# Performance work log

Hardware: AMD Instinct MI355X
Metric: run time of the kernel (lower is better)

The kernel has to match this reference:

```python
import jax, jax.numpy as jnp
import numpy as np

DIM = 1024
NUM_HEADS = 16
HEAD_DIM = DIM // NUM_HEADS
SCALE = HEAD_DIM ** -0.5
CAUSAL = True


def setup_inputs() -> dict:
    key = jax.random.key(0)
    k_x, k_qkv, k_proj, k_pb = jax.random.split(key, 4)
    B, S = 4, 2048
    x = jax.random.normal(k_x, (B, S, DIM), dtype=jnp.float32)
    # nn.Linear(dim, 3*dim, bias=False): weight [3*dim, dim]; store transposed [dim, 3*dim]
    w_qkv = jax.random.normal(k_qkv, (DIM, 3 * DIM), dtype=jnp.float32) * (DIM ** -0.5)
    w_proj = jax.random.normal(k_proj, (DIM, DIM), dtype=jnp.float32) * (DIM ** -0.5)
    b_proj = jax.random.normal(k_pb, (DIM,), dtype=jnp.float32) * 0.01
    return {"x": x, "w_qkv": w_qkv, "w_proj": w_proj, "b_proj": b_proj}


def reference(x, w_qkv, w_proj, b_proj):
    B, S, C = x.shape
    # qkv: [B, S, 3, H, D] -> q,k,v each [B, H, S, D]
    qkv = (x @ w_qkv).reshape(B, S, 3, NUM_HEADS, HEAD_DIM)
    qkv = jnp.transpose(qkv, (2, 0, 3, 1, 4))
    q, k, v = qkv[0], qkv[1], qkv[2]
    # scores [B, H, S, S]
    attn = jnp.einsum('bhqd,bhkd->bhqk', q, k) * SCALE
    if CAUSAL:
        causal_mask = jnp.triu(jnp.ones((S, S), dtype=bool), k=1)
        attn = jnp.where(causal_mask, -jnp.inf, attn)
    attn = jax.nn.softmax(attn, axis=-1)
    out = jnp.einsum('bhqk,bhkd->bhqd', attn, v)
    out = jnp.transpose(out, (0, 2, 1, 3)).reshape(B, S, C)
    return out @ w_proj + b_proj
```

## Files before the change

kernel.cpp:

```cpp
#include <hip/hip_runtime.h>
#include <hip/hip_bf16.h>
#include <math.h>

#define DIMC 1024
#define NHEADS 16
#define HDIM 64
#define BATCH 4
#define SEQ 2048
#define NROWS (BATCH * SEQ)
#define ATTN_SCALE 0.125f
#define LOG2E 1.4426950408889634f

typedef __attribute__((ext_vector_type(8))) short short8;
typedef __attribute__((ext_vector_type(4))) short short4v;
typedef __attribute__((ext_vector_type(4))) float f32x4;

static __device__ __forceinline__ short f2bf(float f) {
    __hip_bfloat16 h = __float2bfloat16(f);
    return *reinterpret_cast<short*>(&h);
}

static __device__ __forceinline__ void gload16(const void* g, void* l) {
    __builtin_amdgcn_global_load_lds(
        (const __attribute__((address_space(1))) unsigned int*)g,
        (__attribute__((address_space(3))) unsigned int*)l, 16, 0, 0);
}

__global__ __launch_bounds__(256)
void xcvt(const float* __restrict__ in, unsigned short* __restrict__ out) {
    int i = blockIdx.x * 256 + threadIdx.x;
    const float4* p = reinterpret_cast<const float4*>(in) + 2 * i;
    float4 a = p[0], b = p[1];
    short8 pk;
    pk[0] = f2bf(a.x); pk[1] = f2bf(a.y); pk[2] = f2bf(a.z); pk[3] = f2bf(a.w);
    pk[4] = f2bf(b.x); pk[5] = f2bf(b.y); pk[6] = f2bf(b.z); pk[7] = f2bf(b.w);
    reinterpret_cast<short8*>(out)[i] = pk;
}

__global__ __launch_bounds__(256)
void transpose_cvt(const float* __restrict__ src, unsigned short* __restrict__ dst,
                   int N) {
    __shared__ float t[64][65];
    const int tid = threadIdx.x;
    const int cb = blockIdx.x * 64;
    const int rb = blockIdx.y * 64;
#pragma unroll
    for (int e = 0; e < 4; e++) {
        int idx = tid + e * 256;
        int row = idx >> 4;
        int c4 = (idx & 15) << 2;
        *reinterpret_cast<float4*>(&t[row][c4]) =
            *reinterpret_cast<const float4*>(&src[(size_t)(rb + row) * N + cb + c4]);
    }
    __syncthreads();
#pragma unroll
    for (int e = 0; e < 2; e++) {
        int idx = tid + e * 256;
        int col = idx >> 3;
        int k8 = (idx & 7) << 3;
        short8 pk;
#pragma unroll
        for (int j = 0; j < 8; j++) pk[j] = f2bf(t[k8 + j][col]);
        *reinterpret_cast<short8*>(&dst[(size_t)(cb + col) * 1024 + rb + k8]) = pk;
    }
}

__global__ __launch_bounds__(256)
void qkv_gemm_mfma(const unsigned short* __restrict__ Xbf,
                   const unsigned short* __restrict__ Wt,
                   unsigned short* __restrict__ qo, unsigned short* __restrict__ ko,
                   unsigned short* __restrict__ vt) {
    __shared__ short Alds[128][32];
    __shared__ short Blds[128][32];
    const int tid = threadIdx.x;
    const int lane = tid & 63;
    const int wave = tid >> 6;
    const int wr = wave >> 1, wc = wave & 1;
    const int rowbase = blockIdx.y * 128;
    const int colbase = blockIdx.x * 128;
    const int g = lane >> 4, li = lane & 15;
    const int srow0 = (wave * 2 + 0) * 16 + (lane >> 2);
    const int srow1 = (wave * 2 + 1) * 16 + (lane >> 2);
    const int scol = (lane & 3) * 8;
    short* aflat = &Alds[0][0];
    short* bflat = &Blds[0][0];

    f32x4 acc[4][4];
#pragma unroll
    for (int m = 0; m < 4; m++)
#pragma unroll
        for (int n = 0; n < 4; n++) acc[m][n] = (f32x4){0.f, 0.f, 0.f, 0.f};

    for (int k0 = 0; k0 < DIMC; k0 += 32) {
        gload16(&Xbf[(size_t)(rowbase + srow0) * DIMC + k0 + scol],
                aflat + (wave * 2 + 0) * 512);
        gload16(&Xbf[(size_t)(rowbase + srow1) * DIMC + k0 + scol],
                aflat + (wave * 2 + 1) * 512);
        gload16(&Wt[(size_t)(colbase + srow0) * 1024 + k0 + scol],
                bflat + (wave * 2 + 0) * 512);
        gload16(&Wt[(size_t)(colbase + srow1) * 1024 + k0 + scol],
                bflat + (wave * 2 + 1) * 512);
        __syncthreads();
        short8 af[4], bfr[4];
#pragma unroll
        for (int m = 0; m < 4; m++)
            af[m] = *reinterpret_cast<const short8*>(&Alds[wr * 64 + m * 16 + li][g * 8]);
#pragma unroll
        for (int n = 0; n < 4; n++)
            bfr[n] = *reinterpret_cast<const short8*>(&Blds[wc * 64 + n * 16 + li][g * 8]);
#pragma unroll
        for (int m = 0; m < 4; m++)
#pragma unroll
            for (int n = 0; n < 4; n++)
                acc[m][n] = __builtin_amdgcn_mfma_f32_16x16x32_bf16(
                    af[m], bfr[n], acc[m][n], 0, 0, 0);
        __syncthreads();
    }

    const int col0 = colbase + wc * 64;
    const int three = col0 >> 10;
    const int h = (col0 & 1023) >> 6;
    if (three < 2) {
        unsigned short* dst = (three == 0) ? qo : ko;
        const float mult = (three == 0) ? (ATTN_SCALE * LOG2E) : 1.0f;
#pragma unroll
        for (int n = 0; n < 4; n++) {
            int d = n * 16 + li;
#pragma unroll
            for (int m = 0; m < 4; m++) {
                int r0 = rowbase + wr * 64 + m * 16 + g * 4;
                int b = r0 >> 11;
                size_t base = ((size_t)(b * NHEADS + h) * SEQ) * HDIM + d;
#pragma unroll
                for (int r = 0; r < 4; r++) {
                    int s = (r0 + r) & 2047;
                    dst[base + (size_t)s * HDIM] = (unsigned short)f2bf(acc[m][n][r] * mult);
                }
            }
        }
    } else {
#pragma unroll
        for (int n = 0; n < 4; n++) {
            int d = n * 16 + li;
#pragma unroll
            for (int m = 0; m < 4; m++) {
                int r0 = rowbase + wr * 64 + m * 16 + g * 4;
                int b = r0 >> 11, s0 = r0 & 2047;
                short4v pk;
#pragma unroll
                for (int r = 0; r < 4; r++) pk[r] = f2bf(acc[m][n][r]);
                *reinterpret_cast<short4v*>(
                    &vt[((size_t)(b * NHEADS + h) * HDIM + d) * SEQ + s0]) = pk;
            }
        }
    }
}

__global__ __launch_bounds__(256)
void proj_gemm_mfma(const unsigned short* __restrict__ Abf,
                    const unsigned short* __restrict__ Wt,
                    const float* __restrict__ bias, float* __restrict__ out) {
    __shared__ short Alds[128][32];
    __shared__ short Blds[128][32];
    const int tid = threadIdx.x;
    const int lane = tid & 63;
    const int wave = tid >> 6;
    const int wr = wave >> 1, wc = wave & 1;
    const int rowbase = blockIdx.y * 128;
    const int colbase = blockIdx.x * 128;
    const int g = lane >> 4, li = lane & 15;
    const int srow0 = (wave * 2 + 0) * 16 + (lane >> 2);
    const int srow1 = (wave * 2 + 1) * 16 + (lane >> 2);
    const int scol = (lane & 3) * 8;
    short* aflat = &Alds[0][0];
    short* bflat = &Blds[0][0];

    f32x4 acc[4][4];
#pragma unroll
    for (int m = 0; m < 4; m++)
#pragma unroll
        for (int n = 0; n < 4; n++) acc[m][n] = (f32x4){0.f, 0.f, 0.f, 0.f};

    for (int k0 = 0; k0 < DIMC; k0 += 32) {
        gload16(&Abf[(size_t)(rowbase + srow0) * DIMC + k0 + scol],
                aflat + (wave * 2 + 0) * 512);
        gload16(&Abf[(size_t)(rowbase + srow1) * DIMC + k0 + scol],
                aflat + (wave * 2 + 1) * 512);
        gload16(&Wt[(size_t)(colbase + srow0) * 1024 + k0 + scol],
                bflat + (wave * 2 + 0) * 512);
        gload16(&Wt[(size_t)(colbase + srow1) * 1024 + k0 + scol],
                bflat + (wave * 2 + 1) * 512);
        __syncthreads();
        short8 af[4], bfr[4];
#pragma unroll
        for (int m = 0; m < 4; m++)
            af[m] = *reinterpret_cast<const short8*>(&Alds[wr * 64 + m * 16 + li][g * 8]);
#pragma unroll
        for (int n = 0; n < 4; n++)
            bfr[n] = *reinterpret_cast<const short8*>(&Blds[wc * 64 + n * 16 + li][g * 8]);
#pragma unroll
        for (int m = 0; m < 4; m++)
#pragma unroll
            for (int n = 0; n < 4; n++)
                acc[m][n] = __builtin_amdgcn_mfma_f32_16x16x32_bf16(
                    af[m], bfr[n], acc[m][n], 0, 0, 0);
        __syncthreads();
    }

#pragma unroll
    for (int n = 0; n < 4; n++) {
        int col = colbase + wc * 64 + n * 16 + li;
        float bv = bias[col];
#pragma unroll
        for (int m = 0; m < 4; m++) {
            int r0 = rowbase + wr * 64 + m * 16 + g * 4;
#pragma unroll
            for (int r = 0; r < 4; r++)
                out[(size_t)(r0 + r) * DIMC + col] = acc[m][n][r] + bv;
        }
    }
}

__global__ __launch_bounds__(256)
void flash_attn_mfma(const unsigned short* __restrict__ qg,
                     const unsigned short* __restrict__ kg,
                     const unsigned short* __restrict__ vt,
                     unsigned short* __restrict__ og) {
    __shared__ short Klds[2][64][64];
    __shared__ short Vlds[2][64][64];
    __shared__ short Plds[4][32][64];
    const int tid = threadIdx.x;
    const int lane = tid & 63;
    const int w = tid >> 6;
    const int g = lane >> 4, li = lane & 15;
    const int sw = li & 7;
    const int orig = blockIdx.x;
    const int swz = (orig & 7) * 64 + (orig >> 3);
    const int bx = swz & 7;
    const int bh = swz >> 3;
    const size_t head = (size_t)bh * SEQ * HDIM;
    const int b = bh >> 4, h = bh & 15;

    const int c0r = tid >> 3, c0c = tid & 7;
    const int c1r = (tid + 256) >> 3, c1c = tid & 7;

    for (int pass = 0; pass < 2; pass++) {
        const int qtile = pass ? (15 - bx) : bx;
        const int qbase = qtile * 128;
        const int qw = qbase + w * 32;
        const int nt = 2 * qtile + 2;

        short8 bq[2][2];
#pragma unroll
        for (int n = 0; n < 2; n++)
#pragma unroll
            for (int ds = 0; ds < 2; ds++)
                bq[n][ds] = *reinterpret_cast<const short8*>(
                    &qg[head + (size_t)(qw + li + 16 * n) * HDIM + ds * 32 + g * 8]);

        f32x4 accO[4][2];
#pragma unroll
        for (int df = 0; df < 4; df++)
#pragma unroll
            for (int n = 0; n < 2; n++) accO[df][n] = (f32x4){0.f, 0.f, 0.f, 0.f};
        float mrow[2] = {-INFINITY, -INFINITY};
        float lrow[2] = {0.f, 0.f};

        short8 kreg0, kreg1, vreg0, vreg1;
        kreg0 = *reinterpret_cast<const short8*>(&kg[head + (size_t)c0r * HDIM + c0c * 8]);
        vreg0 = *reinterpret_cast<const short8*>(&vt[head + (size_t)c0r * SEQ + c0c * 8]);
        kreg1 = *reinterpret_cast<const short8*>(&kg[head + (size_t)c1r * HDIM + c1c * 8]);
        vreg1 = *reinterpret_cast<const short8*>(&vt[head + (size_t)c1r * SEQ + c1c * 8]);
        *reinterpret_cast<short8*>(&Klds[0][c0r][(c0c ^ (c0r & 7)) * 8]) = kreg0;
        *reinterpret_cast<short8*>(&Vlds[0][c0r][(c0c ^ (c0r & 7)) * 8]) = vreg0;
        *reinterpret_cast<short8*>(&Klds[0][c1r][(c1c ^ (c1r & 7)) * 8]) = kreg1;
        *reinterpret_cast<short8*>(&Vlds[0][c1r][(c1c ^ (c1r & 7)) * 8]) = vreg1;
        __syncthreads();

        for (int t = 0; t < nt; t++) {
            const int kvbase = t * 64;
            const int buf = t & 1;
            const bool more = (t + 1 < nt);
            if (more) {
                const int kb2 = kvbase + 64;
                kreg0 = *reinterpret_cast<const short8*>(
                    &kg[head + (size_t)(kb2 + c0r) * HDIM + c0c * 8]);
                vreg0 = *reinterpret_cast<const short8*>(
                    &vt[head + (size_t)c0r * SEQ + kb2 + c0c * 8]);
                kreg1 = *reinterpret_cast<const short8*>(
                    &kg[head + (size_t)(kb2 + c1r) * HDIM + c1c * 8]);
                vreg1 = *reinterpret_cast<const short8*>(
                    &vt[head + (size_t)c1r * SEQ + kb2 + c1c * 8]);
            }

            if (kvbase <= qw + 31) {
                f32x4 s[4][2];
#pragma unroll
                for (int m = 0; m < 4; m++)
#pragma unroll
                    for (int n = 0; n < 2; n++) s[m][n] = (f32x4){0.f, 0.f, 0.f, 0.f};
#pragma unroll
                for (int ds = 0; ds < 2; ds++) {
                    short8 ak[4];
#pragma unroll
                    for (int m = 0; m < 4; m++)
                        ak[m] = *reinterpret_cast<const short8*>(
                            &Klds[buf][li + 16 * m][(((ds * 4 + g) ^ sw)) * 8]);
#pragma unroll
                    for (int m = 0; m < 4; m++)
#pragma unroll
                        for (int n = 0; n < 2; n++)
                            s[m][n] = __builtin_amdgcn_mfma_f32_16x16x32_bf16(
                                ak[m], bq[n][ds], s[m][n], 0, 0, 0);
                }
                const bool diag = (kvbase + 63 > qw);
                float tmax[2] = {-INFINITY, -INFINITY};
#pragma unroll
                for (int n = 0; n < 2; n++) {
                    int q = qw + li + 16 * n;
#pragma unroll
                    for (int m = 0; m < 4; m++) {
#pragma unroll
                        for (int r = 0; r < 4; r++) {
                            if (diag) {
                                int kv = kvbase + 16 * m + 4 * g + r;
                                if (kv > q) s[m][n][r] = -INFINITY;
                            }
                            tmax[n] = fmaxf(tmax[n], s[m][n][r]);
                        }
                    }
                }
                float corr[2];
#pragma unroll
                for (int n = 0; n < 2; n++) {
                    tmax[n] = fmaxf(tmax[n], __shfl_xor(tmax[n], 16));
                    tmax[n] = fmaxf(tmax[n], __shfl_xor(tmax[n], 32));
                    float mnew = fmaxf(mrow[n], tmax[n]);
                    corr[n] = __builtin_amdgcn_exp2f(mrow[n] - mnew);
                    mrow[n] = mnew;
                }
                float tsum[2] = {0.f, 0.f};
#pragma unroll
                for (int m = 0; m < 4; m++) {
#pragma unroll
                    for (int n = 0; n < 2; n++) {
                        float p0 = __builtin_amdgcn_exp2f(s[m][n][0] - mrow[n]);
                        float p1 = __builtin_amdgcn_exp2f(s[m][n][1] - mrow[n]);
                        float p2 = __builtin_amdgcn_exp2f(s[m][n][2] - mrow[n]);
                        float p3 = __builtin_amdgcn_exp2f(s[m][n][3] - mrow[n]);
                        tsum[n] += (p0 + p1) + (p2 + p3);
                        short4v pk;
                        pk[0] = f2bf(p0); pk[1] = f2bf(p1);
                        pk[2] = f2bf(p2); pk[3] = f2bf(p3);
                        *reinterpret_cast<short4v*>(
                            &Plds[w][li + 16 * n]
                                 [((2 * m + (g >> 1)) ^ sw) * 8 + (g & 1) * 4]) = pk;
                    }
                }
#pragma unroll
                for (int n = 0; n < 2; n++) {
                    tsum[n] += __shfl_xor(tsum[n], 16);
                    tsum[n] += __shfl_xor(tsum[n], 32);
                    lrow[n] = lrow[n] * corr[n] + tsum[n];
                }
                bool nore = (corr[0] == 1.0f) && (corr[1] == 1.0f);
                if (!__all((int)nore)) {
#pragma unroll
                    for (int df = 0; df < 4; df++)
#pragma unroll
                        for (int n = 0; n < 2; n++) {
                            accO[df][n][0] *= corr[n]; accO[df][n][1] *= corr[n];
                            accO[df][n][2] *= corr[n]; accO[df][n][3] *= corr[n];
                        }
                }
#pragma unroll
                for (int ks = 0; ks < 2; ks++) {
                    short8 av[4], bp[2];
#pragma unroll
                    for (int df = 0; df < 4; df++)
                        av[df] = *reinterpret_cast<const short8*>(
                            &Vlds[buf][li + 16 * df][((ks * 4 + g) ^ sw) * 8]);
#pragma unroll
                    for (int n = 0; n < 2; n++)
                        bp[n] = *reinterpret_cast<const short8*>(
                            &Plds[w][li + 16 * n][((ks * 4 + g) ^ sw) * 8]);
#pragma unroll
                    for (int df = 0; df < 4; df++)
#pragma unroll
                        for (int n = 0; n < 2; n++)
                            accO[df][n] = __builtin_amdgcn_mfma_f32_16x16x32_bf16(
                                av[df], bp[n], accO[df][n], 0, 0, 0);
                }
            }

            if (more) {
                const int nbuf = buf ^ 1;
                *reinterpret_cast<short8*>(&Klds[nbuf][c0r][(c0c ^ (c0r & 7)) * 8]) = kreg0;
                *reinterpret_cast<short8*>(&Vlds[nbuf][c0r][(c0c ^ (c0r & 7)) * 8]) = vreg0;
                *reinterpret_cast<short8*>(&Klds[nbuf][c1r][(c1c ^ (c1r & 7)) * 8]) = kreg1;
                *reinterpret_cast<short8*>(&Vlds[nbuf][c1r][(c1c ^ (c1r & 7)) * 8]) = vreg1;
            }
            __syncthreads();
        }

#pragma unroll
        for (int n = 0; n < 2; n++) {
            float inv = 1.0f / lrow[n];
            int q = qw + li + 16 * n;
            size_t rowoff = (size_t)(b * SEQ + q) * DIMC + h * HDIM;
#pragma unroll
            for (int df = 0; df < 4; df++) {
                short4v pk;
#pragma unroll
                for (int r = 0; r < 4; r++) pk[r] = f2bf(accO[df][n][r] * inv);
                *reinterpret_cast<short4v*>(&og[rowoff + 16 * df + 4 * g]) = pk;
            }
        }
        __syncthreads();
    }
}

extern "C" void kernel_launch(void* const* d_in, const int* in_sizes, int n_in,
                              void* d_out, int out_size, void* d_ws, size_t ws_size,
                              hipStream_t stream) {
    const float* x      = (const float*)d_in[0];
    const float* w_qkv  = (const float*)d_in[1];
    const float* w_proj = (const float*)d_in[2];
    const float* b_proj = (const float*)d_in[3];
    float* out = (float*)d_out;

    char* w = (char*)d_ws;
    unsigned short* qb  = (unsigned short*)(w);
    unsigned short* kb  = (unsigned short*)(w + ((size_t)16 << 20));
    unsigned short* vtb = (unsigned short*)(w + ((size_t)32 << 20));
    unsigned short* ao  = (unsigned short*)(w + ((size_t)48 << 20));
    unsigned short* wqt = (unsigned short*)(w + ((size_t)64 << 20));
    unsigned short* wpt = (unsigned short*)(w + ((size_t)72 << 20));
    unsigned short* xbf = (unsigned short*)(w + ((size_t)80 << 20));

    xcvt<<<NROWS * DIMC / (256 * 8), 256, 0, stream>>>(x, xbf);
    transpose_cvt<<<dim3(3 * DIMC / 64, DIMC / 64), 256, 0, stream>>>(w_qkv, wqt, 3 * DIMC);
    transpose_cvt<<<dim3(DIMC / 64, DIMC / 64), 256, 0, stream>>>(w_proj, wpt, DIMC);
    qkv_gemm_mfma<<<dim3(3 * DIMC / 128, NROWS / 128), 256, 0, stream>>>(xbf, wqt, qb, kb, vtb);
    flash_attn_mfma<<<512, 256, 0, stream>>>(qb, kb, vtb, ao);
    proj_gemm_mfma<<<dim3(DIMC / 128, NROWS / 128), 256, 0, stream>>>(ao, wpt, b_proj, out);
}
```

Before: 272.0 us.

## Launch one attention block per query tile, heaviest tiles first

Each flash-attention block used to handle a pair of causal query tiles (light plus heavy) in two passes. Now it handles a single query tile, the grid doubles to 1024 blocks, and the order puts the largest causal tiles first so the scheduler can balance load. The change also hoists the causal mask out of the max loop, builds the row max as a tree reduction, truncates P to bf16 with bit masking instead of round-to-nearest, and walks K/V with incremented pointers. The trade-offs are more blocks each reloading their Q tile, reliance on dynamic scheduling to balance the causal work, and slightly different rounding of P.

Measured after the change: 299.6 us. 10.1% more time.

```diff
diff --git a/kernel.cpp b/kernel.cpp
--- a/kernel.cpp
+++ b/kernel.cpp
@@ -235,188 +235,194 @@
     const int g = lane >> 4, li = lane & 15;
     const int sw = li & 7;
     const int orig = blockIdx.x;
-    const int swz = (orig & 7) * 64 + (orig >> 3);
-    const int bx = swz & 7;
-    const int bh = swz >> 3;
+    const int swz = (orig & 7) * 128 + (orig >> 3);
+    const int bh = swz >> 4;
+    const int qtile = 15 - (swz & 15);
     const size_t head = (size_t)bh * SEQ * HDIM;
     const int b = bh >> 4, h = bh & 15;
 
     const int c0r = tid >> 3, c0c = tid & 7;
-    const int c1r = (tid + 256) >> 3, c1c = tid & 7;
-
-    for (int pass = 0; pass < 2; pass++) {
-        const int qtile = pass ? (15 - bx) : bx;
-        const int qbase = qtile * 128;
-        const int qw = qbase + w * 32;
-        const int nt = 2 * qtile + 2;
-
-        short8 bq[2][2];
-#pragma unroll
-        for (int n = 0; n < 2; n++)
-#pragma unroll
-            for (int ds = 0; ds < 2; ds++)
-                bq[n][ds] = *reinterpret_cast<const short8*>(
-                    &qg[head + (size_t)(qw + li + 16 * n) * HDIM + ds * 32 + g * 8]);
-
-        f32x4 accO[4][2];
-#pragma unroll
-        for (int df = 0; df < 4; df++)
-#pragma unroll
-            for (int n = 0; n < 2; n++) accO[df][n] = (f32x4){0.f, 0.f, 0.f, 0.f};
-        float mrow[2] = {-INFINITY, -INFINITY};
-        float lrow[2] = {0.f, 0.f};
-
-        short8 kreg0, kreg1, vreg0, vreg1;
-        kreg0 = *reinterpret_cast<const short8*>(&kg[head + (size_t)c0r * HDIM + c0c * 8]);
-        vreg0 = *reinterpret_cast<const short8*>(&vt[head + (size_t)c0r * SEQ + c0c * 8]);
-        kreg1 = *reinterpret_cast<const short8*>(&kg[head + (size_t)c1r * HDIM + c1c * 8]);
-        vreg1 = *reinterpret_cast<const short8*>(&vt[head + (size_t)c1r * SEQ + c1c * 8]);
-        *reinterpret_cast<short8*>(&Klds[0][c0r][(c0c ^ (c0r & 7)) * 8]) = kreg0;
-        *reinterpret_cast<short8*>(&Vlds[0][c0r][(c0c ^ (c0r & 7)) * 8]) = vreg0;
-        *reinterpret_cast<short8*>(&Klds[0][c1r][(c1c ^ (c1r & 7)) * 8]) = kreg1;
-        *reinterpret_cast<short8*>(&Vlds[0][c1r][(c1c ^ (c1r & 7)) * 8]) = vreg1;
-        __syncthreads();
-
-        for (int t = 0; t < nt; t++) {
-            const int kvbase = t * 64;
-            const int buf = t & 1;
-            const bool more = (t + 1 < nt);
-            if (more) {
-                const int kb2 = kvbase + 64;
-                kreg0 = *reinterpret_cast<const short8*>(
-                    &kg[head + (size_t)(kb2 + c0r) * HDIM + c0c * 8]);
-                vreg0 = *reinterpret_cast<const short8*>(
-                    &vt[head + (size_t)c0r * SEQ + kb2 + c0c * 8]);
-                kreg1 = *reinterpret_cast<const short8*>(
-                    &kg[head + (size_t)(kb2 + c1r) * HDIM + c1c * 8]);
-                vreg1 = *reinterpret_cast<const short8*>(
-                    &vt[head + (size_t)c1r * SEQ + kb2 + c1c * 8]);
-            }
-
-            if (kvbase <= qw + 31) {
-                f32x4 s[4][2];
+
+    const int qbase = qtile * 128;
+    const int qw = qbase + w * 32;
+    const int nt = 2 * qtile + 2;
+
+    short8 bq[2][2];
+#pragma unroll
+    for (int n = 0; n < 2; n++)
+#pragma unroll
+        for (int ds = 0; ds < 2; ds++)
+            bq[n][ds] = *reinterpret_cast<const short8*>(
+                &qg[head + (size_t)(qw + li + 16 * n) * HDIM + ds * 32 + g * 8]);
+
+    f32x4 accO[4][2];
+#pragma unroll
+    for (int df = 0; df < 4; df++)
+#pragma unroll
+        for (int n = 0; n < 2; n++) accO[df][n] = (f32x4){0.f, 0.f, 0.f, 0.f};
+    float mrow[2] = {-INFINITY, -INFINITY};
+    float lrow[2] = {0.f, 0.f};
+
+    const unsigned short* kp = kg + head + (size_t)c0r * HDIM + c0c * 8;
+    const unsigned short* vp = vt + head + (size_t)c0r * SEQ + c0c * 8;
+
+    short8 kreg0, kreg1, vreg0, vreg1;
+    kreg0 = *reinterpret_cast<const short8*>(kp);
+    kreg1 = *reinterpret_cast<const short8*>(kp + 32 * HDIM);
+    vreg0 = *reinterpret_cast<const short8*>(vp);
+    vreg1 = *reinterpret_cast<const short8*>(vp + 32 * SEQ);
+    kp += 64 * HDIM; vp += 64;
+    {
+        const int sw0 = (c0c ^ (c0r & 7)) * 8;
+        const int sw1 = (c0c ^ ((c0r + 32) & 7)) * 8;
+        *reinterpret_cast<short8*>(&Klds[0][c0r][sw0]) = kreg0;
+        *reinterpret_cast<short8*>(&Vlds[0][c0r][sw0]) = vreg0;
+        *reinterpret_cast<short8*>(&Klds[0][c0r + 32][sw1]) = kreg1;
+        *reinterpret_cast<short8*>(&Vlds[0][c0r + 32][sw1]) = vreg1;
+    }
+    __syncthreads();
+
+    for (int t = 0; t < nt; t++) {
+        const int kvbase = t * 64;
+        const int buf = t & 1;
+        const bool more = (t + 1 < nt);
+        if (more) {
+            kreg0 = *reinterpret_cast<const short8*>(kp);
+            kreg1 = *reinterpret_cast<const short8*>(kp + 32 * HDIM);
+            vreg0 = *reinterpret_cast<const short8*>(vp);
+            vreg1 = *reinterpret_cast<const short8*>(vp + 32 * SEQ);
+            kp += 64 * HDIM; vp += 64;
+        }
+
+        if (kvbase <= qw + 31) {
+            f32x4 s[4][2];
+#pragma unroll
+            for (int m = 0; m < 4; m++)
+#pragma unroll
+                for (int n = 0; n < 2; n++) s[m][n] = (f32x4){0.f, 0.f, 0.f, 0.f};
+#pragma unroll
+            for (int ds = 0; ds < 2; ds++) {
+                short8 ak[4];
 #pragma unroll
                 for (int m = 0; m < 4; m++)
-#pragma unroll
-                    for (int n = 0; n < 2; n++) s[m][n] = (f32x4){0.f, 0.f, 0.f, 0.f};
-#pragma unroll
-                for (int ds = 0; ds < 2; ds++) {
-                    short8 ak[4];
-#pragma unroll
-                    for (int m = 0; m < 4; m++)
-                        ak[m] = *reinterpret_cast<const short8*>(
-                            &Klds[buf][li + 16 * m][(((ds * 4 + g) ^ sw)) * 8]);
-#pragma unroll
-                    for (int m = 0; m < 4; m++)
-#pragma unroll
-                        for (int n = 0; n < 2; n++)
-                            s[m][n] = __builtin_amdgcn_mfma_f32_16x16x32_bf16(
-                                ak[m], bq[n][ds], s[m][n], 0, 0, 0);
-                }
-                const bool diag = (kvbase + 63 > qw);
-                float tmax[2] = {-INFINITY, -INFINITY};
+                    ak[m] = *reinterpret_cast<const short8*>(
+                        &Klds[buf][li + 16 * m][(((ds * 4 + g) ^ sw)) * 8]);
+#pragma unroll
+                for (int m = 0; m < 4; m++)
+#pragma unroll
+                    for (int n = 0; n < 2; n++)
+                        s[m][n] = __builtin_amdgcn_mfma_f32_16x16x32_bf16(
+                            ak[m], bq[n][ds], s[m][n], 0, 0, 0);
+            }
+            const bool diag = (kvbase + 63 > qw);
+            if (diag) {
 #pragma unroll
                 for (int n = 0; n < 2; n++) {
                     int q = qw + li + 16 * n;
 #pragma unroll
-                    for (int m = 0; m < 4; m++) {
+                    for (int m = 0; m < 4; m++)
 #pragma unroll
                         for (int r = 0; r < 4; r++) {
-                            if (diag) {
-                                int kv = kvbase + 16 * m + 4 * g + r;
-                                if (kv > q) s[m][n][r] = -INFINITY;
-                            }
-                            tmax[n] = fmaxf(tmax[n], s[m][n][r]);
-                        }
-                    }
-                }
-                float corr[2];
-#pragma unroll
-                for (int n = 0; n < 2; n++) {
-                    tmax[n] = fmaxf(tmax[n], __shfl_xor(tmax[n], 16));
-                    tmax[n] = fmaxf(tmax[n], __shfl_xor(tmax[n], 32));
-                    float mnew = fmaxf(mrow[n], tmax[n]);
-                    corr[n] = __builtin_amdgcn_exp2f(mrow[n] - mnew);
-                    mrow[n] = mnew;
-                }
-                float tsum[2] = {0.f, 0.f};
-#pragma unroll
-                for (int m = 0; m < 4; m++) {
-#pragma unroll
-                    for (int n = 0; n < 2; n++) {
-                        float p0 = __builtin_amdgcn_exp2f(s[m][n][0] - mrow[n]);
-                        float p1 = __builtin_amdgcn_exp2f(s[m][n][1] - mrow[n]);
-                        float p2 = __builtin_amdgcn_exp2f(s[m][n][2] - mrow[n]);
-                        float p3 = __builtin_amdgcn_exp2f(s[m][n][3] - mrow[n]);
-                        tsum[n] += (p0 + p1) + (p2 + p3);
-                        short4v pk;
-                        pk[0] = f2bf(p0); pk[1] = f2bf(p1);
-                        pk[2] = f2bf(p2); pk[3] = f2bf(p3);
-                        *reinterpret_cast<short4v*>(
-                            &Plds[w][li + 16 * n]
-                                 [((2 * m + (g >> 1)) ^ sw) * 8 + (g & 1) * 4]) = pk;
-                    }
-                }
-#pragma unroll
-                for (int n = 0; n < 2; n++) {
-                    tsum[n] += __shfl_xor(tsum[n], 16);
-                    tsum[n] += __shfl_xor(tsum[n], 32);
-                    lrow[n] = lrow[n] * corr[n] + tsum[n];
-                }
-                bool nore = (corr[0] == 1.0f) && (corr[1] == 1.0f);
-                if (!__all((int)nore)) {
-#pragma unroll
-                    for (int df = 0; df < 4; df++)
-#pragma unroll
-                        for (int n = 0; n < 2; n++) {
-                            accO[df][n][0] *= corr[n]; accO[df][n][1] *= corr[n];
-                            accO[df][n][2] *= corr[n]; accO[df][n][3] *= corr[n];
+                            int kv = kvbase + 16 * m + 4 * g + r;
+                            if (kv > q) s[m][n][r] = -INFINITY;
                         }
                 }
-#pragma unroll
-                for (int ks = 0; ks < 2; ks++) {
-                    short8 av[4], bp[2];
-#pragma unroll
-                    for (int df = 0; df < 4; df++)
-                        av[df] = *reinterpret_cast<const short8*>(
-                            &Vlds[buf][li + 16 * df][((ks * 4 + g) ^ sw) * 8]);
+            }
+            float corr[2];
+#pragma unroll
+            for (int n = 0; n < 2; n++) {
+                float a0 = fmaxf(fmaxf(s[0][n][0], s[0][n][1]), fmaxf(s[0][n][2], s[0][n][3]));
+                float a1 = fmaxf(fmaxf(s[1][n][0], s[1][n][1]), fmaxf(s[1][n][2], s[1][n][3]));
+                float a2 = fmaxf(fmaxf(s[2][n][0], s[2][n][1]), fmaxf(s[2][n][2], s[2][n][3]));
+                float a3 = fmaxf(fmaxf(s[3][n][0], s[3][n][1]), fmaxf(s[3][n][2], s[3][n][3]));
+                float tm = fmaxf(fmaxf(a0, a1), fmaxf(a2, a3));
+                tm = fmaxf(tm, __shfl_xor(tm, 16));
+                tm = fmaxf(tm, __shfl_xor(tm, 32));
+                float mnew = fmaxf(mrow[n], tm);
+                corr[n] = __builtin_amdgcn_exp2f(mrow[n] - mnew);
+                mrow[n] = mnew;
+            }
+            float sm[4][2];
+#pragma unroll
+            for (int m = 0; m < 4; m++) {
+#pragma unroll
+                for (int n = 0; n < 2; n++) {
+                    float p0 = __builtin_amdgcn_exp2f(s[m][n][0] - mrow[n]);
+                    float p1 = __builtin_amdgcn_exp2f(s[m][n][1] - mrow[n]);
+                    float p2 = __builtin_amdgcn_exp2f(s[m][n][2] - mrow[n]);
+                    float p3 = __builtin_amdgcn_exp2f(s[m][n][3] - mrow[n]);
+                    sm[m][n] = (p0 + p1) + (p2 + p3);
+                    unsigned u01 = (__float_as_uint(p1) & 0xFFFF0000u) |
+                                   (__float_as_uint(p0) >> 16);
+                    unsigned u23 = (__float_as_uint(p3) & 0xFFFF0000u) |
+                                   (__float_as_uint(p2) >> 16);
+                    *reinterpret_cast<uint2*>(
+                        &Plds[w][li + 16 * n]
+                             [((2 * m + (g >> 1)) ^ sw) * 8 + (g & 1) * 4]) =
+                        make_uint2(u01, u23);
+                }
+            }
+#pragma unroll
+            for (int n = 0; n < 2; n++) {
+                float ts = (sm[0][n] + sm[1][n]) + (sm[2][n] + sm[3][n]);
+                ts += __shfl_xor(ts, 16);
+                ts += __shfl_xor(ts, 32);
+                lrow[n] = lrow[n] * corr[n] + ts;
+            }
+            bool nore = (corr[0] == 1.0f) && (corr[1] == 1.0f);
+            if (!__all((int)nore)) {
+#pragma unroll
+                for (int df = 0; df < 4; df++)
+#pragma unroll
+                    for (int n = 0; n < 2; n++) {
+                        accO[df][n][0] *= corr[n]; accO[df][n][1] *= corr[n];
+                        accO[df][n][2] *= corr[n]; accO[df][n][3] *= corr[n];
+                    }
+            }
+#pragma unroll
+            for (int ks = 0; ks < 2; ks++) {
+                short8 av[4], bp[2];
+#pragma unroll
+                for (int df = 0; df < 4; df++)
+                    av[df] = *reinterpret_cast<const short8*>(
+                        &Vlds[buf][li + 16 * df][((ks * 4 + g) ^ sw) * 8]);
+#pragma unroll
+                for (int n = 0; n < 2; n++)
+                    bp[n] = *reinterpret_cast<const short8*>(
+                        &Plds[w][li + 16 * n][((ks * 4 + g) ^ sw) * 8]);
+#pragma unroll
+                for (int df = 0; df < 4; df++)
 #pragma unroll
                     for (int n = 0; n < 2; n++)
-                        bp[n] = *reinterpret_cast<const short8*>(
-                            &Plds[w][li + 16 * n][((ks * 4 + g) ^ sw) * 8]);
-#pragma unroll
-                    for (int df = 0; df < 4; df++)
-#pragma unroll
-                        for (int n = 0; n < 2; n++)
-                            accO[df][n] = __builtin_amdgcn_mfma_f32_16x16x32_bf16(
-                                av[df], bp[n], accO[df][n], 0, 0, 0);
-                }
-            }
-
-            if (more) {
-                const int nbuf = buf ^ 1;
-                *reinterpret_cast<short8*>(&Klds[nbuf][c0r][(c0c ^ (c0r & 7)) * 8]) = kreg0;
-                *reinterpret_cast<short8*>(&Vlds[nbuf][c0r][(c0c ^ (c0r & 7)) * 8]) = vreg0;
-                *reinterpret_cast<short8*>(&Klds[nbuf][c1r][(c1c ^ (c1r & 7)) * 8]) = kreg1;
-                *reinterpret_cast<short8*>(&Vlds[nbuf][c1r][(c1c ^ (c1r & 7)) * 8]) = vreg1;
-            }
-            __syncthreads();
-        }
-
-#pragma unroll
-        for (int n = 0; n < 2; n++) {
-            float inv = 1.0f / lrow[n];
-            int q = qw + li + 16 * n;
-            size_t rowoff = (size_t)(b * SEQ + q) * DIMC + h * HDIM;
-#pragma unroll
-            for (int df = 0; df < 4; df++) {
-                short4v pk;
-#pragma unroll
-                for (int r = 0; r < 4; r++) pk[r] = f2bf(accO[df][n][r] * inv);
-                *reinterpret_cast<short4v*>(&og[rowoff + 16 * df + 4 * g]) = pk;
-            }
+                        accO[df][n] = __builtin_amdgcn_mfma_f32_16x16x32_bf16(
+                            av[df], bp[n], accO[df][n], 0, 0, 0);
+            }
+        }
+
+        if (more) {
+            const int nbuf = buf ^ 1;
+            const int sw0 = (c0c ^ (c0r & 7)) * 8;
+            const int sw1 = (c0c ^ ((c0r + 32) & 7)) * 8;
+            *reinterpret_cast<short8*>(&Klds[nbuf][c0r][sw0]) = kreg0;
+            *reinterpret_cast<short8*>(&Vlds[nbuf][c0r][sw0]) = vreg0;
+            *reinterpret_cast<short8*>(&Klds[nbuf][c0r + 32][sw1]) = kreg1;
+            *reinterpret_cast<short8*>(&Vlds[nbuf][c0r + 32][sw1]) = vreg1;
         }
         __syncthreads();
+    }
+
+#pragma unroll
+    for (int n = 0; n < 2; n++) {
+        float inv = 1.0f / lrow[n];
+        int q = qw + li + 16 * n;
+        size_t rowoff = (size_t)(b * SEQ + q) * DIMC + h * HDIM;
+#pragma unroll
+        for (int df = 0; df < 4; df++) {
+            short4v pk;
+#pragma unroll
+            for (int r = 0; r < 4; r++) pk[r] = f2bf(accO[df][n][r] * inv);
+            *reinterpret_cast<short4v*>(&og[rowoff + 16 * df + 4 * g]) = pk;
+        }
     }
 }
 
@@ -442,6 +448,6 @@
     transpose_cvt<<<dim3(3 * DIMC / 64, DIMC / 64), 256, 0, stream>>>(w_qkv, wqt, 3 * DIMC);
     transpose_cvt<<<dim3(DIMC / 64, DIMC / 64), 256, 0, stream>>>(w_proj, wpt, DIMC);
     qkv_gemm_mfma<<<dim3(3 * DIMC / 128, NROWS / 128), 256, 0, stream>>>(xbf, wqt, qb, kb, vtb);
-    flash_attn_mfma<<<512, 256, 0, stream>>>(qb, kb, vtb, ao);
+    flash_attn_mfma<<<1024, 256, 0, stream>>>(qb, kb, vtb, ao);
     proj_gemm_mfma<<<dim3(DIMC / 128, NROWS / 128), 256, 0, stream>>>(ao, wpt, b_proj, out);
 }
```
